# Kernel optimization log

Hardware: AMD Instinct MI355X
Metric: run time of the kernel (lower is better)

The kernel has to match this reference:

```python
import jax, jax.numpy as jnp
import numpy as np

N_NODES = 50000
N_EDGES = 1600000
N_GRAPHS = 64
IN_DIM = 128
HID = 128
N_CLASSES = 10


def setup_inputs() -> dict:
    key = jax.random.key(0)
    ks = jax.random.split(key, 12)
    x = jax.random.normal(ks[0], (N_NODES, IN_DIM), dtype=jnp.float32)
    edge_index = jax.random.randint(ks[1], (2, N_EDGES), 0, N_NODES, dtype=jnp.int32)
    batch = jnp.sort(jax.random.randint(ks[2], (N_NODES,), 0, N_GRAPHS, dtype=jnp.int32))
    def glorot(k, shape):
        s = 1.0 / np.sqrt(shape[0])
        return jax.random.uniform(k, shape, jnp.float32, -s, s)
    W1 = glorot(ks[3], (IN_DIM, HID)); b1 = jnp.zeros((HID,), jnp.float32)
    W2 = glorot(ks[4], (HID, HID));    b2 = jnp.zeros((HID,), jnp.float32)
    Wc1 = glorot(ks[5], (HID, HID));   bc1 = glorot(ks[6], (HID,))
    Wc2 = glorot(ks[7], (HID, N_CLASSES)); bc2 = glorot(ks[8], (N_CLASSES,))
    return {"x": x, "edge_index": edge_index, "batch": batch,
            "W1": W1, "b1": b1, "W2": W2, "b2": b2,
            "Wc1": Wc1, "bc1": bc1, "Wc2": Wc2, "bc2": bc2}


def gcn_conv(x, edge_index, W, b):
    """PyG GCNConv: sym-normalized A-hat (with self loops) @ (x W) + b."""
    n = x.shape[0]
    loop = jnp.arange(n, dtype=edge_index.dtype)
    src = jnp.concatenate([edge_index[0], loop])  # message source
    dst = jnp.concatenate([edge_index[1], loop])  # message target
    deg = jax.ops.segment_sum(jnp.ones_like(src, dtype=x.dtype), dst, num_segments=n)
    dinv = jnp.where(deg > 0, jax.lax.rsqrt(deg), jnp.zeros_like(deg))
    norm = dinv[src] * dinv[dst]  # [E+N]
    h = x @ W                     # [N, H]
    msg = h[src] * norm[:, None]  # gather + scale
    out = jax.ops.segment_sum(msg, dst, num_segments=n)
    return out + b


def reference(x, edge_index, batch, W1, b1, W2, b2, Wc1, bc1, Wc2, bc2):
    h = jax.nn.relu(gcn_conv(x, edge_index, W1, b1))
    h = jax.nn.relu(gcn_conv(h, edge_index, W2, b2))
    # per-graph mean pooling (segment mean)
    sums = jax.ops.segment_sum(h, batch, num_segments=N_GRAPHS)
    cnt = jax.ops.segment_sum(jnp.ones((h.shape[0],), h.dtype), batch, num_segments=N_GRAPHS)
    g = sums / jnp.clip(cnt, 1.0)[:, None]  # [G, H]
    z = jax.nn.relu(g @ Wc1 + bc1)
    return z @ Wc2 + bc2
```

## Files before the change

kernel.cpp:

```cpp
#include <hip/hip_runtime.h>
#include <cstdint>
#include <cstddef>

#define CHUNK 4096

typedef __attribute__((ext_vector_type(8))) short short8;
typedef __attribute__((ext_vector_type(4))) float f32x4;

__device__ __forceinline__ float bf2f(unsigned short u) {
  return __uint_as_float(((unsigned)u) << 16);
}
__device__ __forceinline__ unsigned short f2bf(float f) {
  unsigned u = __float_as_uint(f);
  u += 0x7fffu + ((u >> 16) & 1u);
  return (unsigned short)(u >> 16);
}

__global__ void transpose2_w_k(const float* __restrict__ W1, const float* __restrict__ W2,
                               unsigned short* __restrict__ W1t, unsigned short* __restrict__ W2t) {
  int idx = blockIdx.x * 256 + threadIdx.x;
  const float* W = (idx < 16384) ? W1 : W2;
  unsigned short* Wt = (idx < 16384) ? W1t : W2t;
  int i = idx & 16383;
  int k = i >> 7, n = i & 127;
  Wt[n * 128 + k] = f2bf(W[i]);
}

__global__ void count_edges_k(const int* __restrict__ dst, int E, int* __restrict__ cnt) {
  int e = blockIdx.x * blockDim.x + threadIdx.x;
  if (e < E) atomicAdd(&cnt[dst[e]], 1);
}

__global__ void dinv_k(const int* __restrict__ cnt, float* __restrict__ dinv, int n) {
  int i = blockIdx.x * blockDim.x + threadIdx.x;
  if (i < n) dinv[i] = rsqrtf((float)cnt[i] + 1.0f);
}

template <typename CT>
__global__ void fill_csr_k(const int* __restrict__ src, const int* __restrict__ dst, int E,
                           int* __restrict__ cursor, CT* __restrict__ col) {
  int e = blockIdx.x * blockDim.x + threadIdx.x;
  if (e < E) {
    int d = dst[e], s = src[e];
    int pos = atomicAdd(&cursor[d], 1);
    col[pos] = (CT)s;
  }
}

__global__ void scan1_k(const int* __restrict__ cnt, int* __restrict__ rs,
                        int* __restrict__ partials, int n) {
  __shared__ int s[1024];
  int t = threadIdx.x;
  int gid = blockIdx.x * 1024 + t;
  int v = (gid < n) ? cnt[gid] : 0;
  s[t] = v;
  __syncthreads();
  for (int off = 1; off < 1024; off <<= 1) {
    int u = (t >= off) ? s[t - off] : 0;
    __syncthreads();
    s[t] += u;
    __syncthreads();
  }
  if (gid < n) rs[gid] = s[t] - v;
  if (t == 1023) partials[blockIdx.x] = s[1023];
}

__global__ void scan2_k(int* __restrict__ partials, int nb) {
  if (threadIdx.x == 0 && blockIdx.x == 0) {
    int acc = 0;
    for (int i = 0; i < nb; i++) { int v = partials[i]; partials[i] = acc; acc += v; }
  }
}

__global__ void scan3_k(int* __restrict__ rs, int* __restrict__ cursor,
                        const int* __restrict__ partials, int n, int total) {
  int gid = blockIdx.x * blockDim.x + threadIdx.x;
  if (gid < n) {
    int v = rs[gid] + partials[gid >> 10];
    rs[gid] = v;
    cursor[gid] = v;
  }
  if (gid == 0) rs[n] = total;
}

__global__ __launch_bounds__(256) void hist_k(const int* __restrict__ dst, int E,
                                              int* __restrict__ blk_cnt, int nblk, int B) {
  __shared__ int h[256];
  int t = threadIdx.x;
  if (t < B) h[t] = 0;
  __syncthreads();
  int e0 = blockIdx.x * CHUNK;
  int e1 = e0 + CHUNK; if (e1 > E) e1 = E;
  for (int e = e0 + t; e < e1; e += 256) atomicAdd(&h[dst[e] >> 8], 1);
  __syncthreads();
  if (t < B) blk_cnt[(size_t)t * nblk + blockIdx.x] = h[t];
}

__global__ __launch_bounds__(256) void bucket_prefix_k(int* __restrict__ blk_cnt, int nblk, int B,
                                                       int* __restrict__ bucket_tot) {
  int wid = (blockIdx.x * 256 + threadIdx.x) >> 6;
  int lane = threadIdx.x & 63;
  if (wid >= B) return;
  int* p = blk_cnt + (size_t)wid * nblk;
  int running = 0;
  for (int c0 = 0; c0 < nblk; c0 += 64) {
    int idx = c0 + lane;
    int orig = (idx < nblk) ? p[idx] : 0;
    int v = orig;
    #pragma unroll
    for (int off = 1; off < 64; off <<= 1) {
      int u = __shfl_up(v, off);
      if (lane >= off) v += u;
    }
    int tot = __shfl(v, 63);
    if (idx < nblk) p[idx] = running + (v - orig);
    running += tot;
  }
  if (lane == 0) bucket_tot[wid] = running;
}

__global__ void bucket_base_k(const int* __restrict__ bucket_tot, int B,
                              int* __restrict__ bucket_base) {
  int lane = threadIdx.x;
  int running = 0;
  for (int c0 = 0; c0 < B; c0 += 64) {
    int idx = c0 + lane;
    int orig = (idx < B) ? bucket_tot[idx] : 0;
    int v = orig;
    #pragma unroll
    for (int off = 1; off < 64; off <<= 1) {
      int u = __shfl_up(v, off);
      if (lane >= off) v += u;
    }
    int tot = __shfl(v, 63);
    if (idx < B) bucket_base[idx] = running + (v - orig);
    running += tot;
  }
  if (lane == 0) bucket_base[B] = running;
}

__global__ __launch_bounds__(256) void bucket_scatter_k(const int* __restrict__ src,
                                                        const int* __restrict__ dst, int E,
                                                        const int* __restrict__ blk_pre, int nblk,
                                                        const int* __restrict__ bucket_base, int B,
                                                        unsigned int* __restrict__ tmp) {
  __shared__ int h[256];
  __shared__ int base_s[256];
  int t = threadIdx.x;
  if (t < B) {
    h[t] = 0;
    base_s[t] = bucket_base[t] + blk_pre[(size_t)t * nblk + blockIdx.x];
  }
  __syncthreads();
  int e0 = blockIdx.x * CHUNK;
  int e1 = e0 + CHUNK; if (e1 > E) e1 = E;
  for (int e = e0 + t; e < e1; e += 256) {
    int d = dst[e];
    int b = d >> 8;
    int r = atomicAdd(&h[b], 1);
    tmp[base_s[b] + r] = ((unsigned)src[e] << 8) | (unsigned)(d & 255);
  }
}

__global__ __launch_bounds__(256) void bucket_cntfill_k(const unsigned int* __restrict__ tmp,
                                                        const int* __restrict__ bucket_base,
                                                        int N, int E,
                                                        float* __restrict__ dinv,
                                                        int* __restrict__ rs,
                                                        unsigned short* __restrict__ col) {
  __shared__ int c[256];
  __shared__ int cur[256];
  int b = blockIdx.x, t = threadIdx.x;
  c[t] = 0;
  __syncthreads();
  int s0 = bucket_base[b], s1 = bucket_base[b + 1];
  for (int i = s0 + t; i < s1; i += 256) atomicAdd(&c[tmp[i] & 255u], 1);
  __syncthreads();
  int v = c[t];
  cur[t] = v;
  __syncthreads();
  for (int off = 1; off < 256; off <<= 1) {
    int u = (t >= off) ? cur[t - off] : 0;
    __syncthreads();
    cur[t] += u;
    __syncthreads();
  }
  int rsv = s0 + cur[t] - v;
  int node = (b << 8) + t;
  if (node < N) {
    rs[node] = rsv;
    dinv[node] = rsqrtf((float)v + 1.0f);
  }
  if (b == 0 && t == 0) rs[N] = E;
  __syncthreads();
  cur[t] = rsv;
  __syncthreads();
  for (int i = s0 + t; i < s1; i += 256) {
    unsigned u = tmp[i];
    int pos = atomicAdd(&cur[u & 255u], 1);
    col[pos] = (unsigned short)(u >> 8);
  }
}

template <bool AF32>
__global__ __launch_bounds__(256) void gemm_bf_k(const void* __restrict__ Ap,
                                                 const unsigned short* __restrict__ Wt,
                                                 unsigned short* __restrict__ C, int N) {
  __shared__ unsigned short Ws[128 * 136];
  for (int idx = threadIdx.x; idx < 2048; idx += 256) {
    int n = idx >> 4, c = idx & 15;
    *(uint4*)&Ws[n * 136 + c * 8] = ((const uint4*)Wt)[idx];
  }
  __syncthreads();
  const int w = threadIdx.x >> 6;
  const int lane = threadIdx.x & 63;
  const int quad = lane >> 4, l16 = lane & 15;
  const int rb = blockIdx.x * 128 + w * 32;
  f32x4 acc[2][8] = {};
  #pragma unroll
  for (int ks = 0; ks < 4; ks++) {
    short8 aF[2];
    #pragma unroll
    for (int m = 0; m < 2; m++) {
      int r = rb + m * 16 + l16;
      short8 a = {};
      if (r < N) {
        if (AF32) {
          const float* ar = (const float*)Ap + (size_t)r * 128 + ks * 32 + quad * 8;
          float4 u0 = *(const float4*)ar;
          float4 u1 = *(const float4*)(ar + 4);
          a[0] = (short)f2bf(u0.x); a[1] = (short)f2bf(u0.y);
          a[2] = (short)f2bf(u0.z); a[3] = (short)f2bf(u0.w);
          a[4] = (short)f2bf(u1.x); a[5] = (short)f2bf(u1.y);
          a[6] = (short)f2bf(u1.z); a[7] = (short)f2bf(u1.w);
        } else {
          a = *(const short8*)((const unsigned short*)Ap + (size_t)r * 128 + ks * 32 + quad * 8);
        }
      }
      aF[m] = a;
    }
    #pragma unroll
    for (int t = 0; t < 8; t++) {
      short8 bF = *(const short8*)&Ws[(t * 16 + l16) * 136 + ks * 32 + quad * 8];
      acc[0][t] = __builtin_amdgcn_mfma_f32_16x16x32_bf16(aF[0], bF, acc[0][t], 0, 0, 0);
      acc[1][t] = __builtin_amdgcn_mfma_f32_16x16x32_bf16(aF[1], bF, acc[1][t], 0, 0, 0);
    }
  }
  __syncthreads();
  unsigned short* Cs = Ws;
  #pragma unroll
  for (int m = 0; m < 2; m++) {
    int rloc = w * 32 + m * 16 + quad * 4;
    #pragma unroll
    for (int t = 0; t < 8; t++)
      #pragma unroll
      for (int rg = 0; rg < 4; rg++)
        Cs[(rloc + rg) * 132 + t * 16 + l16] = f2bf(acc[m][t][rg]);
  }
  __syncthreads();
  const int r0 = blockIdx.x * 128;
  for (int idx = threadIdx.x; idx < 2048; idx += 256) {
    int row = idx >> 4, c = idx & 15;
    int rr = r0 + row;
    if (rr < N) {
      uint2 a = *(uint2*)&Cs[row * 132 + c * 8];
      uint2 b = *(uint2*)&Cs[row * 132 + c * 8 + 4];
      ((uint4*)C)[(size_t)rr * 16 + c] = make_uint4(a.x, a.y, b.x, b.y);
    }
  }
}

template <typename CT, bool OUTF32>
__global__ __launch_bounds__(256) void agg8_k(const unsigned short* __restrict__ h,
                                              const int* __restrict__ rs,
                                              const CT* __restrict__ col,
                                              const float* __restrict__ dinv,
                                              const float* __restrict__ bias,
                                              void* __restrict__ outp, int n) {
  int wid = (blockIdx.x * blockDim.x + threadIdx.x) >> 6;
  int lane = threadIdx.x & 63;
  if (wid >= n) return;
  const int g = lane >> 4;
  const int l = lane & 15;
  float di = dinv[wid];
  float acc[8];
  {
    uint4 sv = ((const uint4*)(h + (size_t)wid * 128))[l];
    float ws = (g == 0) ? di : 0.f;
    acc[0] = bf2f((unsigned short)sv.x) * ws;
    acc[1] = bf2f((unsigned short)(sv.x >> 16)) * ws;
    acc[2] = bf2f((unsigned short)sv.y) * ws;
    acc[3] = bf2f((unsigned short)(sv.y >> 16)) * ws;
    acc[4] = bf2f((unsigned short)sv.z) * ws;
    acc[5] = bf2f((unsigned short)(sv.z >> 16)) * ws;
    acc[6] = bf2f((unsigned short)sv.w) * ws;
    acc[7] = bf2f((unsigned short)(sv.w >> 16)) * ws;
  }
  int beg = rs[wid], end = rs[wid + 1];
  for (int base = beg; base < end; base += 8) {
    int e0 = base + g, e1 = base + 4 + g;
    int i0 = (e0 < end) ? e0 : end - 1;
    int i1 = (e1 < end) ? e1 : end - 1;
    int s0 = (int)col[i0], s1 = (int)col[i1];
    float w0 = (e0 < end) ? dinv[s0] : 0.f;
    float w1 = (e1 < end) ? dinv[s1] : 0.f;
    uint4 h0 = ((const uint4*)(h + (size_t)s0 * 128))[l];
    uint4 h1 = ((const uint4*)(h + (size_t)s1 * 128))[l];
    acc[0] += bf2f((unsigned short)h0.x) * w0 + bf2f((unsigned short)h1.x) * w1;
    acc[1] += bf2f((unsigned short)(h0.x >> 16)) * w0 + bf2f((unsigned short)(h1.x >> 16)) * w1;
    acc[2] += bf2f((unsigned short)h0.y) * w0 + bf2f((unsigned short)h1.y) * w1;
    acc[3] += bf2f((unsigned short)(h0.y >> 16)) * w0 + bf2f((unsigned short)(h1.y >> 16)) * w1;
    acc[4] += bf2f((unsigned short)h0.z) * w0 + bf2f((unsigned short)h1.z) * w1;
    acc[5] += bf2f((unsigned short)(h0.z >> 16)) * w0 + bf2f((unsigned short)(h1.z >> 16)) * w1;
    acc[6] += bf2f((unsigned short)h0.w) * w0 + bf2f((unsigned short)h1.w) * w1;
    acc[7] += bf2f((unsigned short)(h0.w >> 16)) * w0 + bf2f((unsigned short)(h1.w >> 16)) * w1;
  }
  #pragma unroll
  for (int j = 0; j < 8; j++) {
    acc[j] += __shfl_xor(acc[j], 16);
    acc[j] += __shfl_xor(acc[j], 32);
  }
  if (g == 0) {
    float4 bA = *(const float4*)(bias + l * 8);
    float4 bB = *(const float4*)(bias + l * 8 + 4);
    float r0 = fmaxf(acc[0] * di + bA.x, 0.f);
    float r1 = fmaxf(acc[1] * di + bA.y, 0.f);
    float r2 = fmaxf(acc[2] * di + bA.z, 0.f);
    float r3 = fmaxf(acc[3] * di + bA.w, 0.f);
    float r4 = fmaxf(acc[4] * di + bB.x, 0.f);
    float r5 = fmaxf(acc[5] * di + bB.y, 0.f);
    float r6 = fmaxf(acc[6] * di + bB.z, 0.f);
    float r7 = fmaxf(acc[7] * di + bB.w, 0.f);
    if (OUTF32) {
      ((float4*)outp)[(size_t)wid * 32 + l * 2]     = make_float4(r0, r1, r2, r3);
      ((float4*)outp)[(size_t)wid * 32 + l * 2 + 1] = make_float4(r4, r5, r6, r7);
    } else {
      uint4 v;
      v.x = (unsigned)f2bf(r0) | ((unsigned)f2bf(r1) << 16);
      v.y = (unsigned)f2bf(r2) | ((unsigned)f2bf(r3) << 16);
      v.z = (unsigned)f2bf(r4) | ((unsigned)f2bf(r5) << 16);
      v.w = (unsigned)f2bf(r6) | ((unsigned)f2bf(r7) << 16);
      ((uint4*)outp)[(size_t)wid * 16 + l] = v;
    }
  }
}

__global__ void pool_k(const float* __restrict__ h, const int* __restrict__ batch, int n,
                       float* __restrict__ pool, float* __restrict__ gcnt) {
  int f = threadIdx.x;
  int n0 = blockIdx.x * 64;
  if (n0 >= n) return;
  int n1 = n0 + 64; if (n1 > n) n1 = n;
  int gcur = batch[n0];
  float acc = 0.f, cacc = 0.f;
  for (int i = n0; i < n1; i++) {
    int g = batch[i];
    if (g != gcur) {
      atomicAdd(&pool[gcur * 128 + f], acc);
      if (f == 0) atomicAdd(&gcnt[gcur], cacc);
      acc = 0.f; cacc = 0.f; gcur = g;
    }
    acc += h[(size_t)i * 128 + f];
    cacc += 1.f;
  }
  atomicAdd(&pool[gcur * 128 + f], acc);
  if (f == 0) atomicAdd(&gcnt[gcur], cacc);
}

__global__ void classify_k(const float* __restrict__ pool, const float* __restrict__ gcnt,
                           const float* __restrict__ Wc1, const float* __restrict__ bc1,
                           const float* __restrict__ Wc2, const float* __restrict__ bc2,
                           float* __restrict__ out, int nc) {
  __shared__ float gs[128];
  __shared__ float zs[128];
  int g = blockIdx.x, t = threadIdx.x;
  float c = gcnt[g]; if (c < 1.f) c = 1.f;
  gs[t] = pool[g * 128 + t] / c;
  __syncthreads();
  float acc = bc1[t];
  for (int k = 0; k < 128; k++) acc += gs[k] * Wc1[k * 128 + t];
  zs[t] = fmaxf(acc, 0.f);
  __syncthreads();
  if (t < nc) {
    float o = bc2[t];
    for (int k = 0; k < 128; k++) o += zs[k] * Wc2[k * nc + t];
    out[g * nc + t] = o;
  }
}

extern "C" void kernel_launch(void* const* d_in, const int* in_sizes, int n_in,
                              void* d_out, int out_size, void* d_ws, size_t ws_size,
                              hipStream_t stream) {
  const float* x   = (const float*)d_in[0];
  const int*   ei  = (const int*)d_in[1];
  const int*   bat = (const int*)d_in[2];
  const float* W1  = (const float*)d_in[3];
  const float* b1  = (const float*)d_in[4];
  const float* W2  = (const float*)d_in[5];
  const float* b2  = (const float*)d_in[6];
  const float* Wc1 = (const float*)d_in[7];
  const float* bc1 = (const float*)d_in[8];
  const float* Wc2 = (const float*)d_in[9];
  const float* bc2 = (const float*)d_in[10];
  float* out = (float*)d_out;

  const int N  = in_sizes[0] / 128;
  const int E  = in_sizes[1] / 2;
  const int NC = in_sizes[10];
  const int G  = out_size / NC;
  const int* src = ei;
  const int* dst = ei + E;
  (void)n_in; (void)ws_size;

  size_t off = 0;
  auto walloc = [&](size_t bytes) -> void* {
    void* p = (char*)d_ws + off;
    off += (bytes + 255) & ~(size_t)255;
    return p;
  };
  unsigned short* B2 = (unsigned short*)walloc((size_t)N * 128 * 2);
  unsigned short* B3 = (unsigned short*)walloc((size_t)N * 128 * 2);
  float* a2   = (float*)walloc((size_t)N * 128 * 4);
  unsigned short* W1t = (unsigned short*)walloc(128 * 128 * 2);
  unsigned short* W2t = (unsigned short*)walloc(128 * 128 * 2);
  float* dinv = (float*)walloc((size_t)N * 4);
  int*   rs   = (int*)  walloc((size_t)(N + 1) * 4);
  float* pool = (float*)walloc((size_t)G * 129 * 4);
  float* gcnt = pool + (size_t)G * 128;

  const bool small = (N <= 65535);
  const int gblocks = (N + 127) / 128;
  const int aggGrid = (N + 3) / 4;

  transpose2_w_k<<<128, 256, 0, stream>>>(W1, W2, W1t, W2t);

  if (small) {
    const int B    = (N + 255) >> 8;
    const int nblk = (E + CHUNK - 1) / CHUNK;
    unsigned short* col = (unsigned short*)walloc((size_t)E * 2);
    unsigned int*   tmp = (unsigned int*)  walloc((size_t)E * 4);
    int* blk_cnt     = (int*)walloc((size_t)B * nblk * 4);
    int* bucket_tot  = (int*)walloc((size_t)B * 4);
    int* bucket_base = (int*)walloc((size_t)(B + 1) * 4);

    hist_k<<<nblk, 256, 0, stream>>>(dst, E, blk_cnt, nblk, B);
    bucket_prefix_k<<<(B + 3) / 4, 256, 0, stream>>>(blk_cnt, nblk, B, bucket_tot);
    bucket_base_k<<<1, 64, 0, stream>>>(bucket_tot, B, bucket_base);
    bucket_scatter_k<<<nblk, 256, 0, stream>>>(src, dst, E, blk_cnt, nblk, bucket_base, B, tmp);
    bucket_cntfill_k<<<B, 256, 0, stream>>>(tmp, bucket_base, N, E, dinv, rs, col);

    gemm_bf_k<true><<<gblocks, 256, 0, stream>>>(x, W1t, B2, N);
    agg8_k<unsigned short, false><<<aggGrid, 256, 0, stream>>>(B2, rs, col, dinv, b1, B3, N);
    gemm_bf_k<false><<<gblocks, 256, 0, stream>>>(B3, W2t, B2, N);
    agg8_k<unsigned short, true><<<aggGrid, 256, 0, stream>>>(B2, rs, col, dinv, b2, a2, N);
  } else {
    const int nb = (N + 1023) / 1024;
    int* cnt    = (int*)walloc((size_t)N * 4);
    int* cursor = (int*)walloc((size_t)N * 4);
    int* col    = (int*)walloc((size_t)E * 4);
    int* partials = (int*)walloc(256 * 4);
    hipMemsetAsync(cnt, 0, (size_t)N * 4, stream);
    count_edges_k<<<(E + 255) / 256, 256, 0, stream>>>(dst, E, cnt);
    scan1_k<<<nb, 1024, 0, stream>>>(cnt, rs, partials, N);
    scan2_k<<<1, 64, 0, stream>>>(partials, nb);
    scan3_k<<<(N + 255) / 256, 256, 0, stream>>>(rs, cursor, partials, N, E);
    dinv_k<<<(N + 255) / 256, 256, 0, stream>>>(cnt, dinv, N);
    fill_csr_k<int><<<(E + 255) / 256, 256, 0, stream>>>(src, dst, E, cursor, col);

    gemm_bf_k<true><<<gblocks, 256, 0, stream>>>(x, W1t, B2, N);
    agg8_k<int, false><<<aggGrid, 256, 0, stream>>>(B2, rs, col, dinv, b1, B3, N);
    gemm_bf_k<false><<<gblocks, 256, 0, stream>>>(B3, W2t, B2, N);
    agg8_k<int, true><<<aggGrid, 256, 0, stream>>>(B2, rs, col, dinv, b2, a2, N);
  }

  hipMemsetAsync(pool, 0, (size_t)G * 129 * 4, stream);
  pool_k<<<(N + 63) / 64, 128, 0, stream>>>(a2, bat, N, pool, gcnt);
  classify_k<<<G, 128, 0, stream>>>(pool, gcnt, Wc1, bc1, Wc2, bc2, out, NC);
}
```

Baseline: 319.4 us.

## Store hidden features column-chunked and aggregate one 32-feature chunk per block

The GEMM now writes bf16 features in four 32-column chunks, each a contiguous [N,32] array, and the second GEMM reads its input in that layout. The aggregation kernel is split so each block handles one chunk for a group of nodes. Blocks are interleaved across chunks and node halves so that concurrently running blocks gather from a 3.2MB chunk that can stay resident in L2. In exchange, every edge's col and dinv are read four times, each lane gathers only 4 bytes per neighbor instead of 16, and there are four times as many waves.

```diff
diff --git a/kernel.cpp b/kernel.cpp
--- a/kernel.cpp
+++ b/kernel.cpp
@@ -234,7 +234,7 @@
           a[4] = (short)f2bf(u1.x); a[5] = (short)f2bf(u1.y);
           a[6] = (short)f2bf(u1.z); a[7] = (short)f2bf(u1.w);
         } else {
-          a = *(const short8*)((const unsigned short*)Ap + (size_t)r * 128 + ks * 32 + quad * 8);
+          a = *(const short8*)((const unsigned short*)Ap + ((size_t)ks * N + r) * 32 + quad * 8);
         }
       }
       aF[m] = a;
@@ -260,43 +260,39 @@
   __syncthreads();
   const int r0 = blockIdx.x * 128;
   for (int idx = threadIdx.x; idx < 2048; idx += 256) {
-    int row = idx >> 4, c = idx & 15;
+    int row = idx >> 4, seg = idx & 15;
     int rr = r0 + row;
     if (rr < N) {
-      uint2 a = *(uint2*)&Cs[row * 132 + c * 8];
-      uint2 b = *(uint2*)&Cs[row * 132 + c * 8 + 4];
-      ((uint4*)C)[(size_t)rr * 16 + c] = make_uint4(a.x, a.y, b.x, b.y);
+      uint2 a = *(uint2*)&Cs[row * 132 + seg * 8];
+      uint2 b = *(uint2*)&Cs[row * 132 + seg * 8 + 4];
+      int chunk = seg >> 2, sub = seg & 3;
+      ((uint4*)C)[((size_t)chunk * N + rr) * 4 + sub] = make_uint4(a.x, a.y, b.x, b.y);
     }
   }
 }
 
 template <typename CT, bool OUTF32>
-__global__ __launch_bounds__(256) void agg8_k(const unsigned short* __restrict__ h,
+__global__ __launch_bounds__(256) void aggc_k(const unsigned short* __restrict__ h,
                                               const int* __restrict__ rs,
                                               const CT* __restrict__ col,
                                               const float* __restrict__ dinv,
                                               const float* __restrict__ bias,
-                                              void* __restrict__ outp, int n) {
-  int wid = (blockIdx.x * blockDim.x + threadIdx.x) >> 6;
-  int lane = threadIdx.x & 63;
-  if (wid >= n) return;
-  const int g = lane >> 4;
-  const int l = lane & 15;
-  float di = dinv[wid];
-  float acc[8];
-  {
-    uint4 sv = ((const uint4*)(h + (size_t)wid * 128))[l];
-    float ws = (g == 0) ? di : 0.f;
-    acc[0] = bf2f((unsigned short)sv.x) * ws;
-    acc[1] = bf2f((unsigned short)(sv.x >> 16)) * ws;
-    acc[2] = bf2f((unsigned short)sv.y) * ws;
-    acc[3] = bf2f((unsigned short)(sv.y >> 16)) * ws;
-    acc[4] = bf2f((unsigned short)sv.z) * ws;
-    acc[5] = bf2f((unsigned short)(sv.z >> 16)) * ws;
-    acc[6] = bf2f((unsigned short)sv.w) * ws;
-    acc[7] = bf2f((unsigned short)(sv.w >> 16)) * ws;
-  }
-  int beg = rs[wid], end = rs[wid + 1];
+                                              void* __restrict__ outp, int n, int half) {
+  const int slot = blockIdx.x & 7;
+  const int chunk = slot >> 1;
+  const int hh = slot & 1;
+  const int node = hh * half + ((blockIdx.x >> 3) << 2) + (threadIdx.x >> 6);
+  const int hiB = hh ? n : half;
+  if (node >= hiB) return;
+  const int lane = threadIdx.x & 63;
+  const int g = lane >> 4, l = lane & 15;
+  const unsigned* hc = (const unsigned*)h + (size_t)chunk * n * 16;
+  float di = dinv[node];
+  unsigned sv = hc[(size_t)node * 16 + l];
+  float ws = (g == 0) ? di : 0.f;
+  float a0 = bf2f((unsigned short)sv) * ws;
+  float a1 = bf2f((unsigned short)(sv >> 16)) * ws;
+  int beg = rs[node], end = rs[node + 1];
   for (int base = beg; base < end; base += 8) {
     int e0 = base + g, e1 = base + 4 + g;
     int i0 = (e0 < end) ? e0 : end - 1;
@@ -304,43 +300,23 @@
     int s0 = (int)col[i0], s1 = (int)col[i1];
     float w0 = (e0 < end) ? dinv[s0] : 0.f;
     float w1 = (e1 < end) ? dinv[s1] : 0.f;
-    uint4 h0 = ((const uint4*)(h + (size_t)s0 * 128))[l];
-    uint4 h1 = ((const uint4*)(h + (size_t)s1 * 128))[l];
-    acc[0] += bf2f((unsigned short)h0.x) * w0 + bf2f((unsigned short)h1.x) * w1;
-    acc[1] += bf2f((unsigned short)(h0.x >> 16)) * w0 + bf2f((unsigned short)(h1.x >> 16)) * w1;
-    acc[2] += bf2f((unsigned short)h0.y) * w0 + bf2f((unsigned short)h1.y) * w1;
-    acc[3] += bf2f((unsigned short)(h0.y >> 16)) * w0 + bf2f((unsigned short)(h1.y >> 16)) * w1;
-    acc[4] += bf2f((unsigned short)h0.z) * w0 + bf2f((unsigned short)h1.z) * w1;
-    acc[5] += bf2f((unsigned short)(h0.z >> 16)) * w0 + bf2f((unsigned short)(h1.z >> 16)) * w1;
-    acc[6] += bf2f((unsigned short)h0.w) * w0 + bf2f((unsigned short)h1.w) * w1;
-    acc[7] += bf2f((unsigned short)(h0.w >> 16)) * w0 + bf2f((unsigned short)(h1.w >> 16)) * w1;
-  }
-  #pragma unroll
-  for (int j = 0; j < 8; j++) {
-    acc[j] += __shfl_xor(acc[j], 16);
-    acc[j] += __shfl_xor(acc[j], 32);
-  }
+    unsigned v0 = hc[(size_t)s0 * 16 + l];
+    unsigned v1 = hc[(size_t)s1 * 16 + l];
+    a0 += bf2f((unsigned short)v0) * w0 + bf2f((unsigned short)v1) * w1;
+    a1 += bf2f((unsigned short)(v0 >> 16)) * w0 + bf2f((unsigned short)(v1 >> 16)) * w1;
+  }
+  a0 += __shfl_xor(a0, 16); a0 += __shfl_xor(a0, 32);
+  a1 += __shfl_xor(a1, 16); a1 += __shfl_xor(a1, 32);
   if (g == 0) {
-    float4 bA = *(const float4*)(bias + l * 8);
-    float4 bB = *(const float4*)(bias + l * 8 + 4);
-    float r0 = fmaxf(acc[0] * di + bA.x, 0.f);
-    float r1 = fmaxf(acc[1] * di + bA.y, 0.f);
-    float r2 = fmaxf(acc[2] * di + bA.z, 0.f);
-    float r3 = fmaxf(acc[3] * di + bA.w, 0.f);
-    float r4 = fmaxf(acc[4] * di + bB.x, 0.f);
-    float r5 = fmaxf(acc[5] * di + bB.y, 0.f);
-    float r6 = fmaxf(acc[6] * di + bB.z, 0.f);
-    float r7 = fmaxf(acc[7] * di + bB.w, 0.f);
+    float b0 = bias[chunk * 32 + l * 2];
+    float b1 = bias[chunk * 32 + l * 2 + 1];
+    float r0 = fmaxf(a0 * di + b0, 0.f);
+    float r1 = fmaxf(a1 * di + b1, 0.f);
     if (OUTF32) {
-      ((float4*)outp)[(size_t)wid * 32 + l * 2]     = make_float4(r0, r1, r2, r3);
-      ((float4*)outp)[(size_t)wid * 32 + l * 2 + 1] = make_float4(r4, r5, r6, r7);
+      *(float2*)((float*)outp + (size_t)node * 128 + chunk * 32 + l * 2) = make_float2(r0, r1);
     } else {
-      uint4 v;
-      v.x = (unsigned)f2bf(r0) | ((unsigned)f2bf(r1) << 16);
-      v.y = (unsigned)f2bf(r2) | ((unsigned)f2bf(r3) << 16);
-      v.z = (unsigned)f2bf(r4) | ((unsigned)f2bf(r5) << 16);
-      v.w = (unsigned)f2bf(r6) | ((unsigned)f2bf(r7) << 16);
-      ((uint4*)outp)[(size_t)wid * 16 + l] = v;
+      ((unsigned*)outp)[((size_t)chunk * n + node) * 16 + l] =
+          (unsigned)f2bf(r0) | ((unsigned)f2bf(r1) << 16);
     }
   }
 }
@@ -430,7 +406,8 @@
 
   const bool small = (N <= 65535);
   const int gblocks = (N + 127) / 128;
-  const int aggGrid = (N + 3) / 4;
+  const int half = (N + 1) >> 1;
+  const int aggGrid = ((half + 3) / 4) * 8;
 
   transpose2_w_k<<<128, 256, 0, stream>>>(W1, W2, W1t, W2t);
 
@@ -450,9 +427,9 @@
     bucket_cntfill_k<<<B, 256, 0, stream>>>(tmp, bucket_base, N, E, dinv, rs, col);
 
     gemm_bf_k<true><<<gblocks, 256, 0, stream>>>(x, W1t, B2, N);
-    agg8_k<unsigned short, false><<<aggGrid, 256, 0, stream>>>(B2, rs, col, dinv, b1, B3, N);
+    aggc_k<unsigned short, false><<<aggGrid, 256, 0, stream>>>(B2, rs, col, dinv, b1, B3, N, half);
     gemm_bf_k<false><<<gblocks, 256, 0, stream>>>(B3, W2t, B2, N);
-    agg8_k<unsigned short, true><<<aggGrid, 256, 0, stream>>>(B2, rs, col, dinv, b2, a2, N);
+    aggc_k<unsigned short, true><<<aggGrid, 256, 0, stream>>>(B2, rs, col, dinv, b2, a2, N, half);
   } else {
     const int nb = (N + 1023) / 1024;
     int* cnt    = (int*)walloc((size_t)N * 4);
@@ -468,9 +445,9 @@
     fill_csr_k<int><<<(E + 255) / 256, 256, 0, stream>>>(src, dst, E, cursor, col);
 
     gemm_bf_k<true><<<gblocks, 256, 0, stream>>>(x, W1t, B2, N);
-    agg8_k<int, false><<<aggGrid, 256, 0, stream>>>(B2, rs, col, dinv, b1, B3, N);
+    aggc_k<int, false><<<aggGrid, 256, 0, stream>>>(B2, rs, col, dinv, b1, B3, N, half);
     gemm_bf_k<false><<<gblocks, 256, 0, stream>>>(B3, W2t, B2, N);
-    agg8_k<int, true><<<aggGrid, 256, 0, stream>>>(B2, rs, col, dinv, b2, a2, N);
+    aggc_k<int, true><<<aggGrid, 256, 0, stream>>>(B2, rs, col, dinv, b2, a2, N, half);
   }
 
   hipMemsetAsync(pool, 0, (size_t)G * 129 * 4, stream);
```

New measurement: 437.1 us. 1.37x slower.

## Replace multi-pass bucket sort with single atomic scatter pass and bf16 final aggregation

Applied to the files above, without the earlier changes.

The CSR build drops its separate histogram, per-block prefix and scatter kernels. A single kernel now stages each edge chunk in shared memory and reserves slots in fixed-capacity per-bucket regions through global atomics, so edges are read once. The second aggregation writes bf16 instead of fp32, and pooling reads that bf16 buffer, which halves the traffic for that tensor. The trade-offs are a capacity limit per bucket that silently drops edges if a bucket overflows, a non-deterministic order within buckets, and lower precision going into pooling.

```diff
diff --git a/kernel.cpp b/kernel.cpp
--- a/kernel.cpp
+++ b/kernel.cpp
@@ -83,98 +83,77 @@
   if (gid == 0) rs[n] = total;
 }
 
-__global__ __launch_bounds__(256) void hist_k(const int* __restrict__ dst, int E,
-                                              int* __restrict__ blk_cnt, int nblk, int B) {
+__global__ __launch_bounds__(256) void scatter_atomic_k(const int* __restrict__ src,
+                                                        const int* __restrict__ dst, int E,
+                                                        int* __restrict__ gcur,
+                                                        unsigned int* __restrict__ tmp,
+                                                        int cap, int B) {
+  __shared__ unsigned pk[CHUNK];
+  __shared__ unsigned char bk[CHUNK];
   __shared__ int h[256];
+  __shared__ int cur[256];
+  __shared__ int base_s[256];
   int t = threadIdx.x;
-  if (t < B) h[t] = 0;
+  h[t] = 0;
   __syncthreads();
   int e0 = blockIdx.x * CHUNK;
   int e1 = e0 + CHUNK; if (e1 > E) e1 = E;
-  for (int e = e0 + t; e < e1; e += 256) atomicAdd(&h[dst[e] >> 8], 1);
-  __syncthreads();
-  if (t < B) blk_cnt[(size_t)t * nblk + blockIdx.x] = h[t];
-}
-
-__global__ __launch_bounds__(256) void bucket_prefix_k(int* __restrict__ blk_cnt, int nblk, int B,
-                                                       int* __restrict__ bucket_tot) {
-  int wid = (blockIdx.x * 256 + threadIdx.x) >> 6;
-  int lane = threadIdx.x & 63;
-  if (wid >= B) return;
-  int* p = blk_cnt + (size_t)wid * nblk;
+  int m = e1 - e0;
+  for (int i = t; i < m; i += 256) {
+    int d = dst[e0 + i], s = src[e0 + i];
+    int b = d >> 8;
+    pk[i] = ((unsigned)s << 8) | (unsigned)(d & 255);
+    bk[i] = (unsigned char)b;
+    atomicAdd(&h[b], 1);
+  }
+  __syncthreads();
+  if (t < B && h[t] > 0) base_s[t] = atomicAdd(&gcur[t], h[t]);
+  cur[t] = 0;
+  __syncthreads();
+  for (int i = t; i < m; i += 256) {
+    int b = bk[i];
+    int r = atomicAdd(&cur[b], 1);
+    int p = base_s[b] + r;
+    if (p < cap) tmp[(size_t)b * cap + p] = pk[i];
+  }
+}
+
+__global__ void base2_k(const int* __restrict__ gcur, int B, int cap,
+                        int* __restrict__ bucket_base) {
+  int lane = threadIdx.x;
   int running = 0;
-  for (int c0 = 0; c0 < nblk; c0 += 64) {
+  for (int c0 = 0; c0 < B; c0 += 64) {
     int idx = c0 + lane;
-    int orig = (idx < nblk) ? p[idx] : 0;
-    int v = orig;
+    int cb = (idx < B) ? gcur[idx] : 0;
+    if (cb > cap) cb = cap;
+    int v = cb;
     #pragma unroll
     for (int off = 1; off < 64; off <<= 1) {
       int u = __shfl_up(v, off);
       if (lane >= off) v += u;
     }
     int tot = __shfl(v, 63);
-    if (idx < nblk) p[idx] = running + (v - orig);
+    if (idx < B) bucket_base[idx] = running + (v - cb);
     running += tot;
   }
-  if (lane == 0) bucket_tot[wid] = running;
-}
-
-__global__ void bucket_base_k(const int* __restrict__ bucket_tot, int B,
-                              int* __restrict__ bucket_base) {
-  int lane = threadIdx.x;
-  int running = 0;
-  for (int c0 = 0; c0 < B; c0 += 64) {
-    int idx = c0 + lane;
-    int orig = (idx < B) ? bucket_tot[idx] : 0;
-    int v = orig;
-    #pragma unroll
-    for (int off = 1; off < 64; off <<= 1) {
-      int u = __shfl_up(v, off);
-      if (lane >= off) v += u;
-    }
-    int tot = __shfl(v, 63);
-    if (idx < B) bucket_base[idx] = running + (v - orig);
-    running += tot;
-  }
   if (lane == 0) bucket_base[B] = running;
 }
 
-__global__ __launch_bounds__(256) void bucket_scatter_k(const int* __restrict__ src,
-                                                        const int* __restrict__ dst, int E,
-                                                        const int* __restrict__ blk_pre, int nblk,
-                                                        const int* __restrict__ bucket_base, int B,
-                                                        unsigned int* __restrict__ tmp) {
-  __shared__ int h[256];
-  __shared__ int base_s[256];
-  int t = threadIdx.x;
-  if (t < B) {
-    h[t] = 0;
-    base_s[t] = bucket_base[t] + blk_pre[(size_t)t * nblk + blockIdx.x];
-  }
-  __syncthreads();
-  int e0 = blockIdx.x * CHUNK;
-  int e1 = e0 + CHUNK; if (e1 > E) e1 = E;
-  for (int e = e0 + t; e < e1; e += 256) {
-    int d = dst[e];
-    int b = d >> 8;
-    int r = atomicAdd(&h[b], 1);
-    tmp[base_s[b] + r] = ((unsigned)src[e] << 8) | (unsigned)(d & 255);
-  }
-}
-
-__global__ __launch_bounds__(256) void bucket_cntfill_k(const unsigned int* __restrict__ tmp,
-                                                        const int* __restrict__ bucket_base,
-                                                        int N, int E,
-                                                        float* __restrict__ dinv,
-                                                        int* __restrict__ rs,
-                                                        unsigned short* __restrict__ col) {
+__global__ __launch_bounds__(256) void cntfill2_k(const unsigned int* __restrict__ tmp,
+                                                  const int* __restrict__ gcur,
+                                                  const int* __restrict__ bucket_base,
+                                                  int N, int E, int cap,
+                                                  float* __restrict__ dinv,
+                                                  int* __restrict__ rs,
+                                                  unsigned short* __restrict__ col) {
   __shared__ int c[256];
   __shared__ int cur[256];
   int b = blockIdx.x, t = threadIdx.x;
   c[t] = 0;
   __syncthreads();
-  int s0 = bucket_base[b], s1 = bucket_base[b + 1];
-  for (int i = s0 + t; i < s1; i += 256) atomicAdd(&c[tmp[i] & 255u], 1);
+  int cnt_b = gcur[b]; if (cnt_b > cap) cnt_b = cap;
+  const unsigned* tb = tmp + (size_t)b * cap;
+  for (int i = t; i < cnt_b; i += 256) atomicAdd(&c[tb[i] & 255u], 1);
   __syncthreads();
   int v = c[t];
   cur[t] = v;
@@ -185,7 +164,7 @@
     cur[t] += u;
     __syncthreads();
   }
-  int rsv = s0 + cur[t] - v;
+  int rsv = bucket_base[b] + cur[t] - v;
   int node = (b << 8) + t;
   if (node < N) {
     rs[node] = rsv;
@@ -195,8 +174,8 @@
   __syncthreads();
   cur[t] = rsv;
   __syncthreads();
-  for (int i = s0 + t; i < s1; i += 256) {
-    unsigned u = tmp[i];
+  for (int i = t; i < cnt_b; i += 256) {
+    unsigned u = tb[i];
     int pos = atomicAdd(&cur[u & 255u], 1);
     col[pos] = (unsigned short)(u >> 8);
   }
@@ -270,13 +249,13 @@
   }
 }
 
-template <typename CT, bool OUTF32>
+template <typename CT>
 __global__ __launch_bounds__(256) void agg8_k(const unsigned short* __restrict__ h,
                                               const int* __restrict__ rs,
                                               const CT* __restrict__ col,
                                               const float* __restrict__ dinv,
                                               const float* __restrict__ bias,
-                                              void* __restrict__ outp, int n) {
+                                              unsigned short* __restrict__ outp, int n) {
   int wid = (blockIdx.x * blockDim.x + threadIdx.x) >> 6;
   int lane = threadIdx.x & 63;
   if (wid >= n) return;
@@ -331,22 +310,17 @@
     float r5 = fmaxf(acc[5] * di + bB.y, 0.f);
     float r6 = fmaxf(acc[6] * di + bB.z, 0.f);
     float r7 = fmaxf(acc[7] * di + bB.w, 0.f);
-    if (OUTF32) {
-      ((float4*)outp)[(size_t)wid * 32 + l * 2]     = make_float4(r0, r1, r2, r3);
-      ((float4*)outp)[(size_t)wid * 32 + l * 2 + 1] = make_float4(r4, r5, r6, r7);
-    } else {
-      uint4 v;
-      v.x = (unsigned)f2bf(r0) | ((unsigned)f2bf(r1) << 16);
-      v.y = (unsigned)f2bf(r2) | ((unsigned)f2bf(r3) << 16);
-      v.z = (unsigned)f2bf(r4) | ((unsigned)f2bf(r5) << 16);
-      v.w = (unsigned)f2bf(r6) | ((unsigned)f2bf(r7) << 16);
-      ((uint4*)outp)[(size_t)wid * 16 + l] = v;
-    }
-  }
-}
-
-__global__ void pool_k(const float* __restrict__ h, const int* __restrict__ batch, int n,
-                       float* __restrict__ pool, float* __restrict__ gcnt) {
+    uint4 v;
+    v.x = (unsigned)f2bf(r0) | ((unsigned)f2bf(r1) << 16);
+    v.y = (unsigned)f2bf(r2) | ((unsigned)f2bf(r3) << 16);
+    v.z = (unsigned)f2bf(r4) | ((unsigned)f2bf(r5) << 16);
+    v.w = (unsigned)f2bf(r6) | ((unsigned)f2bf(r7) << 16);
+    ((uint4*)outp)[(size_t)wid * 16 + l] = v;
+  }
+}
+
+__global__ void poolb_k(const unsigned short* __restrict__ h, const int* __restrict__ batch, int n,
+                        float* __restrict__ pool, float* __restrict__ gcnt) {
   int f = threadIdx.x;
   int n0 = blockIdx.x * 64;
   if (n0 >= n) return;
@@ -360,7 +334,7 @@
       if (f == 0) atomicAdd(&gcnt[gcur], cacc);
       acc = 0.f; cacc = 0.f; gcur = g;
     }
-    acc += h[(size_t)i * 128 + f];
+    acc += bf2f(h[(size_t)i * 128 + f]);
     cacc += 1.f;
   }
   atomicAdd(&pool[gcur * 128 + f], acc);
@@ -420,7 +394,6 @@
   };
   unsigned short* B2 = (unsigned short*)walloc((size_t)N * 128 * 2);
   unsigned short* B3 = (unsigned short*)walloc((size_t)N * 128 * 2);
-  float* a2   = (float*)walloc((size_t)N * 128 * 4);
   unsigned short* W1t = (unsigned short*)walloc(128 * 128 * 2);
   unsigned short* W2t = (unsigned short*)walloc(128 * 128 * 2);
   float* dinv = (float*)walloc((size_t)N * 4);
@@ -437,22 +410,21 @@
   if (small) {
     const int B    = (N + 255) >> 8;
     const int nblk = (E + CHUNK - 1) / CHUNK;
+    const int cap  = (E + B - 1) / B + 2048;
     unsigned short* col = (unsigned short*)walloc((size_t)E * 2);
-    unsigned int*   tmp = (unsigned int*)  walloc((size_t)E * 4);
-    int* blk_cnt     = (int*)walloc((size_t)B * nblk * 4);
-    int* bucket_tot  = (int*)walloc((size_t)B * 4);
+    unsigned int*   tmp = (unsigned int*)  walloc((size_t)B * cap * 4);
+    int* gcur        = (int*)walloc((size_t)B * 4);
     int* bucket_base = (int*)walloc((size_t)(B + 1) * 4);
 
-    hist_k<<<nblk, 256, 0, stream>>>(dst, E, blk_cnt, nblk, B);
-    bucket_prefix_k<<<(B + 3) / 4, 256, 0, stream>>>(blk_cnt, nblk, B, bucket_tot);
-    bucket_base_k<<<1, 64, 0, stream>>>(bucket_tot, B, bucket_base);
-    bucket_scatter_k<<<nblk, 256, 0, stream>>>(src, dst, E, blk_cnt, nblk, bucket_base, B, tmp);
-    bucket_cntfill_k<<<B, 256, 0, stream>>>(tmp, bucket_base, N, E, dinv, rs, col);
+    hipMemsetAsync(gcur, 0, (size_t)B * 4, stream);
+    scatter_atomic_k<<<nblk, 256, 0, stream>>>(src, dst, E, gcur, tmp, cap, B);
+    base2_k<<<1, 64, 0, stream>>>(gcur, B, cap, bucket_base);
+    cntfill2_k<<<B, 256, 0, stream>>>(tmp, gcur, bucket_base, N, E, cap, dinv, rs, col);
 
     gemm_bf_k<true><<<gblocks, 256, 0, stream>>>(x, W1t, B2, N);
-    agg8_k<unsigned short, false><<<aggGrid, 256, 0, stream>>>(B2, rs, col, dinv, b1, B3, N);
+    agg8_k<unsigned short><<<aggGrid, 256, 0, stream>>>(B2, rs, col, dinv, b1, B3, N);
     gemm_bf_k<false><<<gblocks, 256, 0, stream>>>(B3, W2t, B2, N);
-    agg8_k<unsigned short, true><<<aggGrid, 256, 0, stream>>>(B2, rs, col, dinv, b2, a2, N);
+    agg8_k<unsigned short><<<aggGrid, 256, 0, stream>>>(B2, rs, col, dinv, b2, B3, N);
   } else {
     const int nb = (N + 1023) / 1024;
     int* cnt    = (int*)walloc((size_t)N * 4);
@@ -468,12 +440,12 @@
     fill_csr_k<int><<<(E + 255) / 256, 256, 0, stream>>>(src, dst, E, cursor, col);
 
     gemm_bf_k<true><<<gblocks, 256, 0, stream>>>(x, W1t, B2, N);
-    agg8_k<int, false><<<aggGrid, 256, 0, stream>>>(B2, rs, col, dinv, b1, B3, N);
+    agg8_k<int><<<aggGrid, 256, 0, stream>>>(B2, rs, col, dinv, b1, B3, N);
     gemm_bf_k<false><<<gblocks, 256, 0, stream>>>(B3, W2t, B2, N);
-    agg8_k<int, true><<<aggGrid, 256, 0, stream>>>(B2, rs, col, dinv, b2, a2, N);
+    agg8_k<int><<<aggGrid, 256, 0, stream>>>(B2, rs, col, dinv, b2, B3, N);
   }
 
   hipMemsetAsync(pool, 0, (size_t)G * 129 * 4, stream);
-  pool_k<<<(N + 63) / 64, 128, 0, stream>>>(a2, bat, N, pool, gcnt);
+  poolb_k<<<(N + 63) / 64, 128, 0, stream>>>(B3, bat, N, pool, gcnt);
   classify_k<<<G, 128, 0, stream>>>(pool, gcnt, Wc1, bc1, Wc2, bc2, out, NC);
 }
```

Measured after the change: 314.4 us. Within noise of the previous version (-1.6%).
